# Kernel tuning notes

Hardware: AMD Instinct MI355X
Metric: run time of the kernel (lower is better)

## Reference

```python
import jax, jax.numpy as jnp
import numpy as np

H_SP, W_SP = 8, 8
NUM_HEADS = 6
SHARED = 96
DIM_Q, DIM_KV = 96, 192
WIN = H_SP * W_SP  # 64 tokens per window


def _rel_index():
    # Swin-style relative position index, static numpy computation
    coords = np.stack(np.meshgrid(np.arange(H_SP), np.arange(W_SP), indexing='ij'))
    cf = coords.reshape(2, -1)                      # [2, 64]
    rel = cf[:, :, None] - cf[:, None, :]           # [2, 64, 64]
    rel = rel.transpose(1, 2, 0).astype(np.int64)   # [64, 64, 2]
    rel[..., 0] += H_SP - 1
    rel[..., 1] += W_SP - 1
    rel[..., 0] *= 2 * W_SP - 1
    return rel.sum(-1)                              # [64, 64], values in [0, 225)

REL_IDX = jnp.asarray(_rel_index())


def setup_inputs() -> dict:
    key = jax.random.key(0)
    ks = jax.random.split(key, 12)
    B, H, W = 4, 256, 256
    f32 = jnp.float32
    std = 0.02
    return {
        'x_q':  jax.random.normal(ks[0], (B, DIM_Q, H, W), f32),
        'x_kv': jax.random.normal(ks[1], (B, DIM_KV, H, W), f32),
        'Wq': jax.random.normal(ks[2], (DIM_Q, SHARED), f32) * std,
        'bq': jnp.zeros((SHARED,), f32),
        'Wk': jax.random.normal(ks[3], (DIM_KV, SHARED), f32) * std,
        'bk': jnp.zeros((SHARED,), f32),
        'Wv': jax.random.normal(ks[4], (DIM_KV, SHARED), f32) * std,
        'bv': jnp.zeros((SHARED,), f32),
        'bias_table': jax.random.normal(ks[5], ((2 * H_SP - 1) * (2 * W_SP - 1), NUM_HEADS), f32) * std,
        'Wo': jax.random.normal(ks[6], (SHARED, DIM_Q), f32) * std,
        'bo': jnp.zeros((DIM_Q,), f32),
    }


def reference(x_q, x_kv, Wq, bq, Wk, bk, Wv, bv, bias_table, Wo, bo):
    B, Cq, H, W = x_q.shape
    nH, nW = H // H_SP, W // W_SP  # H, W divisible by window -> pad is a no-op
    hd = SHARED // NUM_HEADS
    scale = hd ** -0.5

    def to_windows(img):
        C = img.shape[1]
        x = img.reshape(B, C, nH, H_SP, nW, W_SP)
        return x.transpose(0, 2, 4, 3, 5, 1).reshape(-1, WIN, C)

    qw = to_windows(x_q)    # [nWin, 64, Cq]
    kvw = to_windows(x_kv)  # [nWin, 64, Ckv]

    def heads(x):
        return x.reshape(-1, WIN, NUM_HEADS, hd).transpose(0, 2, 1, 3)  # [nWin, h, 64, hd]

    q = heads(qw @ Wq + bq)
    k = heads(kvw @ Wk + bk)
    v = heads(kvw @ Wv + bv)

    attn = jnp.einsum('whqd,whkd->whqk', q, k) * scale  # [nWin, h, 64, 64]
    rel_bias = bias_table[REL_IDX].transpose(2, 0, 1)   # [h, 64, 64]
    attn = jax.nn.softmax(attn + rel_bias[None], axis=-1)

    out = jnp.einsum('whqk,whkd->whqd', attn, v)        # [nWin, h, 64, hd]
    out = out.transpose(0, 2, 1, 3).reshape(-1, WIN, SHARED)
    out = out @ Wo + bo                                 # [nWin, 64, Cq]

    # windows2img
    out = out.reshape(B, nH, nW, H_SP, W_SP, Cq)
    out = out.transpose(0, 1, 3, 2, 4, 5).reshape(B, H, W, Cq)
    return out.transpose(0, 3, 1, 2)  # [B, Cq, H, W]
```

## Files before the change

kernel.cpp:

```cpp
#include <hip/hip_runtime.h>

typedef short short8 __attribute__((ext_vector_type(8)));
typedef float f32x4 __attribute__((ext_vector_type(4)));
typedef unsigned short ushort;

#define MFMA(a, b, c) __builtin_amdgcn_mfma_f32_16x16x32_bf16(a, b, c, 0, 0, 0)

#define WS_WQT 0
#define WS_WKT 9216
#define WS_WVT 27648
#define WS_WOT 46080
#define WS_BIAS 55296
#define WS_TOTAL 56646

#define STR_A 104
#define OFF_A 0
#define OFF_K16 13312
#define OFF_VT 25600
#define STR_VT 72
#define OFF_PQ 39424
#define P_STRIDE 72
#define OFF_BIAS 50688
#define LDS_BYTES 53392

__device__ __forceinline__ ushort f2bf(float x) {
    unsigned u = __float_as_uint(x);
    u = (u + 0x7FFFu + ((u >> 16) & 1u)) >> 16;
    return (ushort)u;
}
__device__ __forceinline__ float bf2f(ushort u) {
    return __uint_as_float(((unsigned)u) << 16);
}

__global__ void prep_weights(const float* __restrict__ Wq, const float* __restrict__ Wk,
                             const float* __restrict__ Wv, const float* __restrict__ Wo,
                             const float* __restrict__ btab, ushort* __restrict__ ws) {
    int idx = blockIdx.x * 256 + threadIdx.x;
    if (idx < WS_WKT) {
        int f = idx >> 9, w = idx & 511, lane = w >> 3, j = w & 7;
        int nt = f / 3, kt = f % 3;
        int n = nt * 16 + (lane & 15), k = kt * 32 + (lane >> 4) * 8 + j;
        ws[idx] = f2bf(Wq[k * 96 + n]);
    } else if (idx < WS_WVT) {
        int t = idx - WS_WKT;
        int f = t >> 9, w = t & 511, lane = w >> 3, j = w & 7;
        int kt6 = f / 6, nt = f % 6;
        int n = nt * 16 + (lane & 15), k = kt6 * 32 + (lane >> 4) * 8 + j;
        ws[idx] = f2bf(Wk[k * 96 + n]);
    } else if (idx < WS_WOT) {
        int t = idx - WS_WVT;
        int f = t >> 9, w = t & 511, lane = w >> 3, j = w & 7;
        int kt6 = f / 6, nt = f % 6;
        int n = nt * 16 + (lane & 15), k = kt6 * 32 + (lane >> 4) * 8 + j;
        ws[idx] = f2bf(Wv[k * 96 + n]);
    } else if (idx < WS_BIAS) {
        int t = idx - WS_WOT;
        int f = t >> 9, w = t & 511, lane = w >> 3, j = w & 7;
        int nt = f / 3, kt = f % 3;
        int n = nt * 16 + (lane & 15), k = kt * 32 + (lane >> 4) * 8 + j;
        ws[idx] = f2bf(Wo[k * 96 + n]);
    } else if (idx < WS_TOTAL) {
        ws[idx] = f2bf(btab[idx - WS_BIAS]);
    }
}

__global__ __launch_bounds__(256, 3) void swin_attn(
    const float* __restrict__ xq, const float* __restrict__ xkv,
    const float* __restrict__ bq, const float* __restrict__ bk,
    const float* __restrict__ bv, const float* __restrict__ bo,
    const ushort* __restrict__ ws, float* __restrict__ out)
{
    __shared__ __align__(16) char smem[LDS_BYTES];
    const int tid = threadIdx.x;
    const int wave = tid >> 6, lane = tid & 63;
    const int l15 = lane & 15, quad = lane >> 4;
    int wid = ((blockIdx.x & 7) << 9) | (blockIdx.x >> 3);
    const int b = wid >> 10;
    const int wh = (wid >> 5) & 31, ww = wid & 31;
    const int h0 = wh * 8, w0 = ww * 8;
    const int mt = wave;

    ushort* A     = (ushort*)(smem + OFF_A);
    ushort* k16   = (ushort*)(smem + OFF_K16);
    ushort* vt    = (ushort*)(smem + OFF_VT);
    ushort* ps    = (ushort*)(smem + OFF_PQ) + wave * (16 * P_STRIDE);
    ushort* qsc   = (ushort*)(smem + OFF_PQ + 9216) + wave * 256;
    ushort* biasl = (ushort*)(smem + OFF_BIAS);

    float bqr[6], bkr[6], bvr[6], bor[6];
    #pragma unroll
    for (int h = 0; h < 6; ++h) {
        bqr[h] = bq[h * 16 + l15]; bkr[h] = bk[h * 16 + l15];
        bvr[h] = bv[h * 16 + l15]; bor[h] = bo[h * 16 + l15];
    }

    int pc[3], pi[3];
    #pragma unroll
    for (int t = 0; t < 3; ++t) { int p = tid + t * 256; pc[t] = p % 96; pi[t] = p / 96; }

    const float* xkvb = xkv + (size_t)b * 192 * 65536;
    float4 pf[3][2];
    #pragma unroll
    for (int t = 0; t < 3; ++t) {
        const float* g = xkvb + (size_t)pc[t] * 65536 + (h0 + pi[t]) * 256 + w0;
        pf[t][0] = *(const float4*)g; pf[t][1] = *(const float4*)(g + 4);
    }
    for (int i = tid; i < 1350; i += 256) biasl[i] = ws[WS_BIAS + i];

    #pragma unroll
    for (int t = 0; t < 3; ++t) {
        int base = (pi[t] * 8) * STR_A + pc[t];
        A[base]             = f2bf(pf[t][0].x); A[base + STR_A]     = f2bf(pf[t][0].y);
        A[base + 2 * STR_A] = f2bf(pf[t][0].z); A[base + 3 * STR_A] = f2bf(pf[t][0].w);
        A[base + 4 * STR_A] = f2bf(pf[t][1].x); A[base + 5 * STR_A] = f2bf(pf[t][1].y);
        A[base + 6 * STR_A] = f2bf(pf[t][1].z); A[base + 7 * STR_A] = f2bf(pf[t][1].w);
    }
    __syncthreads();

    float4 pg[3][2];
    #pragma unroll
    for (int t = 0; t < 3; ++t) {
        const float* g = xkvb + (size_t)(96 + pc[t]) * 65536 + (h0 + pi[t]) * 256 + w0;
        pg[t][0] = *(const float4*)g; pg[t][1] = *(const float4*)(g + 4);
    }

    f32x4 accK[6], accV[6];
    #pragma unroll
    for (int n = 0; n < 6; ++n) { accK[n] = {}; accV[n] = {}; }
    const int arow = (mt * 16 + l15) * STR_A + quad * 8;
    #pragma unroll
    for (int kt = 0; kt < 3; ++kt) {
        short8 a = *(const short8*)(A + arow + kt * 32);
        #pragma unroll
        for (int nt = 0; nt < 6; ++nt) {
            short8 bk8 = *(const short8*)(ws + WS_WKT + (((kt * 6) + nt) * 64 + lane) * 8);
            accK[nt] = MFMA(a, bk8, accK[nt]);
            short8 bv8 = *(const short8*)(ws + WS_WVT + (((kt * 6) + nt) * 64 + lane) * 8);
            accV[nt] = MFMA(a, bv8, accV[nt]);
        }
    }
    __syncthreads();

    #pragma unroll
    for (int t = 0; t < 3; ++t) {
        int base = (pi[t] * 8) * STR_A + pc[t];
        A[base]             = f2bf(pg[t][0].x); A[base + STR_A]     = f2bf(pg[t][0].y);
        A[base + 2 * STR_A] = f2bf(pg[t][0].z); A[base + 3 * STR_A] = f2bf(pg[t][0].w);
        A[base + 4 * STR_A] = f2bf(pg[t][1].x); A[base + 5 * STR_A] = f2bf(pg[t][1].y);
        A[base + 6 * STR_A] = f2bf(pg[t][1].z); A[base + 7 * STR_A] = f2bf(pg[t][1].w);
    }
    __syncthreads();

    const float* xqb = xq + (size_t)b * 96 * 65536;
    #pragma unroll
    for (int t = 0; t < 3; ++t) {
        const float* g = xqb + (size_t)pc[t] * 65536 + (h0 + pi[t]) * 256 + w0;
        pf[t][0] = *(const float4*)g; pf[t][1] = *(const float4*)(g + 4);
    }

    #pragma unroll
    for (int kt = 0; kt < 3; ++kt) {
        short8 a = *(const short8*)(A + arow + kt * 32);
        #pragma unroll
        for (int nt = 0; nt < 6; ++nt) {
            short8 bk8 = *(const short8*)(ws + WS_WKT + ((((3 + kt) * 6) + nt) * 64 + lane) * 8);
            accK[nt] = MFMA(a, bk8, accK[nt]);
            short8 bv8 = *(const short8*)(ws + WS_WVT + ((((3 + kt) * 6) + nt) * 64 + lane) * 8);
            accV[nt] = MFMA(a, bv8, accV[nt]);
        }
    }
    #pragma unroll
    for (int nt = 0; nt < 6; ++nt) {
        ushort* dk = k16 + nt * (64 * 16) + (mt * 16 + quad * 4) * 16 + l15;
        ushort* dv = vt + nt * (16 * STR_VT) + l15 * STR_VT + (mt * 16 + quad * 4);
        #pragma unroll
        for (int r = 0; r < 4; ++r) {
            dk[r * 16] = f2bf(accK[nt][r] + bkr[nt]);
            dv[r]      = f2bf(accV[nt][r] + bvr[nt]);
        }
    }
    __syncthreads();

    #pragma unroll
    for (int t = 0; t < 3; ++t) {
        int base = (pi[t] * 8) * STR_A + pc[t];
        A[base]             = f2bf(pf[t][0].x); A[base + STR_A]     = f2bf(pf[t][0].y);
        A[base + 2 * STR_A] = f2bf(pf[t][0].z); A[base + 3 * STR_A] = f2bf(pf[t][0].w);
        A[base + 4 * STR_A] = f2bf(pf[t][1].x); A[base + 5 * STR_A] = f2bf(pf[t][1].y);
        A[base + 6 * STR_A] = f2bf(pf[t][1].z); A[base + 7 * STR_A] = f2bf(pf[t][1].w);
    }
    __syncthreads();

    const int qtok0 = mt * 16 + quad * 4;
    int bidx[4][4];
    #pragma unroll
    for (int nt = 0; nt < 4; ++nt) {
        int kt2 = nt * 16 + l15, i2 = kt2 >> 3, j2 = kt2 & 7;
        #pragma unroll
        for (int r = 0; r < 4; ++r) {
            int qt = qtok0 + r, i1 = qt >> 3, j1 = qt & 7;
            bidx[nt][r] = ((i1 - i2 + 7) * 15 + (j1 - j2 + 7)) * 6;
        }
    }

    f32x4 accO[6];
    short8 zero8 = {};
    for (int h = 0; h < 6; ++h) {
        f32x4 qa = {};
        #pragma unroll
        for (int kt = 0; kt < 3; ++kt) {
            short8 a  = *(const short8*)(A + arow + kt * 32);
            short8 bb = *(const short8*)(ws + WS_WQT + ((h * 3 + kt) * 64 + lane) * 8);
            qa = MFMA(a, bb, qa);
        }
        #pragma unroll
        for (int r = 0; r < 4; ++r)
            qsc[(quad * 4 + r) * 16 + l15] = f2bf((qa[r] + bqr[h]) * 0.25f);

        short8 aq = zero8;
        if (quad < 2) aq = *(const short8*)(qsc + l15 * 16 + quad * 8);
        f32x4 s[4];
        #pragma unroll
        for (int nt = 0; nt < 4; ++nt) {
            short8 bk8 = zero8;
            if (quad < 2) bk8 = *(const short8*)(k16 + h * (64 * 16) + (nt * 16 + l15) * 16 + quad * 8);
            f32x4 z = {};
            s[nt] = MFMA(aq, bk8, z);
        }
        #pragma unroll
        for (int nt = 0; nt < 4; ++nt)
            #pragma unroll
            for (int r = 0; r < 4; ++r)
                s[nt][r] += bf2f(biasl[bidx[nt][r] + h]);
        float pr[4][4];
        #pragma unroll
        for (int r = 0; r < 4; ++r) {
            float m = fmaxf(fmaxf(s[0][r], s[1][r]), fmaxf(s[2][r], s[3][r]));
            m = fmaxf(m, __shfl_xor(m, 1)); m = fmaxf(m, __shfl_xor(m, 2));
            m = fmaxf(m, __shfl_xor(m, 4)); m = fmaxf(m, __shfl_xor(m, 8));
            float l = 0.f;
            #pragma unroll
            for (int nt = 0; nt < 4; ++nt) { pr[nt][r] = __expf(s[nt][r] - m); l += pr[nt][r]; }
            l += __shfl_xor(l, 1); l += __shfl_xor(l, 2);
            l += __shfl_xor(l, 4); l += __shfl_xor(l, 8);
            float inv = 1.0f / l;
            #pragma unroll
            for (int nt = 0; nt < 4; ++nt) pr[nt][r] *= inv;
        }
        #pragma unroll
        for (int nt = 0; nt < 4; ++nt)
            #pragma unroll
            for (int r = 0; r < 4; ++r)
                ps[(quad * 4 + r) * P_STRIDE + nt * 16 + l15] = f2bf(pr[nt][r]);
        f32x4 o = {};
        #pragma unroll
        for (int k2 = 0; k2 < 2; ++k2) {
            short8 ap  = *(const short8*)(ps + l15 * P_STRIDE + k2 * 32 + quad * 8);
            short8 bv8 = *(const short8*)(vt + h * (16 * STR_VT) + l15 * STR_VT + k2 * 32 + quad * 8);
            o = MFMA(ap, bv8, o);
        }
        accO[h] = o;
    }
    __syncthreads();

    ushort* obuf = A;
    #pragma unroll
    for (int h = 0; h < 6; ++h)
        #pragma unroll
        for (int r = 0; r < 4; ++r)
            obuf[(mt * 16 + quad * 4 + r) * STR_A + h * 16 + l15] = f2bf(accO[h][r]);

    {
        int t0 = mt * 16 + quad * 4;
        int i = t0 >> 3, j0 = t0 & 7;
        #pragma unroll
        for (int nt = 0; nt < 6; ++nt) {
            f32x4 acc = {};
            #pragma unroll
            for (int kt = 0; kt < 3; ++kt) {
                short8 a  = *(const short8*)(obuf + arow + kt * 32);
                short8 bb = *(const short8*)(ws + WS_WOT + ((nt * 3 + kt) * 64 + lane) * 8);
                acc = MFMA(a, bb, acc);
            }
            int cout = nt * 16 + l15;
            float4 v4 = make_float4(acc[0] + bor[nt], acc[1] + bor[nt], acc[2] + bor[nt], acc[3] + bor[nt]);
            float* dst = out + (size_t)(b * 96 + cout) * 65536 + (h0 + i) * 256 + w0 + j0;
            *(float4*)dst = v4;
        }
    }
}

extern "C" void kernel_launch(void* const* d_in, const int* in_sizes, int n_in,
                              void* d_out, int out_size, void* d_ws, size_t ws_size,
                              hipStream_t stream) {
    const float* xq   = (const float*)d_in[0];
    const float* xkv  = (const float*)d_in[1];
    const float* Wq   = (const float*)d_in[2];
    const float* bq   = (const float*)d_in[3];
    const float* Wk   = (const float*)d_in[4];
    const float* bk   = (const float*)d_in[5];
    const float* Wv   = (const float*)d_in[6];
    const float* bv   = (const float*)d_in[7];
    const float* btab = (const float*)d_in[8];
    const float* Wo   = (const float*)d_in[9];
    const float* bo   = (const float*)d_in[10];
    ushort* ws = (ushort*)d_ws;
    float* out = (float*)d_out;

    hipLaunchKernelGGL(prep_weights, dim3((WS_TOTAL + 255) / 256), dim3(256), 0, stream,
                       Wq, Wk, Wv, Wo, btab, ws);
    hipLaunchKernelGGL(swin_attn, dim3(4096), dim3(256), 0, stream,
                       xq, xkv, bq, bk, bv, bo, ws, out);
}
```

Baseline: 507.7 us.

## Compute Q projection first into registers and shrink LDS to raise occupancy

Reorders the per-window pipeline so the Q projection is done first and held packed in registers. K is then stored in the reused A buffer rather than a separate K tile, which cuts LDS per block from about 53 KB to about 39 KB, and launch bounds are raised to 4 blocks per CU. Biases are folded into the MFMA accumulator initialisation, softmax reductions use DPP instead of shuffles, and rcp replaces the division. The costs are 12 extra live registers for the packed Q under a tighter register budget, and more bank pressure on the strided K reads.

```diff
diff --git a/kernel.cpp b/kernel.cpp
--- a/kernel.cpp
+++ b/kernel.cpp
@@ -14,14 +14,14 @@
 #define WS_TOTAL 56646
 
 #define STR_A 104
-#define OFF_A 0
-#define OFF_K16 13312
-#define OFF_VT 25600
+#define U_A    0
+#define U_VT   6656
 #define STR_VT 72
-#define OFF_PQ 39424
-#define P_STRIDE 72
-#define OFF_BIAS 50688
-#define LDS_BYTES 53392
+#define U_PS   13568
+#define U_BIAS 18176
+#define U_TOTAL 19526
+
+#define DPP_F(v, ctrl) __int_as_float(__builtin_amdgcn_update_dpp(0, __float_as_int(v), ctrl, 0xF, 0xF, true))
 
 __device__ __forceinline__ ushort f2bf(float x) {
     unsigned u = __float_as_uint(x);
@@ -64,13 +64,13 @@
     }
 }
 
-__global__ __launch_bounds__(256, 3) void swin_attn(
+__global__ __launch_bounds__(256, 4) void swin_attn(
     const float* __restrict__ xq, const float* __restrict__ xkv,
     const float* __restrict__ bq, const float* __restrict__ bk,
     const float* __restrict__ bv, const float* __restrict__ bo,
     const ushort* __restrict__ ws, float* __restrict__ out)
 {
-    __shared__ __align__(16) char smem[LDS_BYTES];
+    __shared__ __align__(16) ushort smem[U_TOTAL + 8];
     const int tid = threadIdx.x;
     const int wave = tid >> 6, lane = tid & 63;
     const int l15 = lane & 15, quad = lane >> 4;
@@ -80,29 +80,27 @@
     const int h0 = wh * 8, w0 = ww * 8;
     const int mt = wave;
 
-    ushort* A     = (ushort*)(smem + OFF_A);
-    ushort* k16   = (ushort*)(smem + OFF_K16);
-    ushort* vt    = (ushort*)(smem + OFF_VT);
-    ushort* ps    = (ushort*)(smem + OFF_PQ) + wave * (16 * P_STRIDE);
-    ushort* qsc   = (ushort*)(smem + OFF_PQ + 9216) + wave * 256;
-    ushort* biasl = (ushort*)(smem + OFF_BIAS);
-
-    float bqr[6], bkr[6], bvr[6], bor[6];
+    ushort* A     = smem + U_A;
+    ushort* vt    = smem + U_VT;
+    ushort* ps    = smem + U_PS + wave * 1152;
+    ushort* qsc   = ps;
+    ushort* biasl = smem + U_BIAS;
+
+    float bqr[6], bkr[6], bvr[6];
     #pragma unroll
     for (int h = 0; h < 6; ++h) {
-        bqr[h] = bq[h * 16 + l15]; bkr[h] = bk[h * 16 + l15];
-        bvr[h] = bv[h * 16 + l15]; bor[h] = bo[h * 16 + l15];
+        bqr[h] = bq[h * 16 + l15]; bkr[h] = bk[h * 16 + l15]; bvr[h] = bv[h * 16 + l15];
     }
 
     int pc[3], pi[3];
     #pragma unroll
     for (int t = 0; t < 3; ++t) { int p = tid + t * 256; pc[t] = p % 96; pi[t] = p / 96; }
 
-    const float* xkvb = xkv + (size_t)b * 192 * 65536;
+    const float* xqb = xq + (size_t)b * 96 * 65536;
     float4 pf[3][2];
     #pragma unroll
     for (int t = 0; t < 3; ++t) {
-        const float* g = xkvb + (size_t)pc[t] * 65536 + (h0 + pi[t]) * 256 + w0;
+        const float* g = xqb + (size_t)pc[t] * 65536 + (h0 + pi[t]) * 256 + w0;
         pf[t][0] = *(const float4*)g; pf[t][1] = *(const float4*)(g + 4);
     }
     for (int i = tid; i < 1350; i += 256) biasl[i] = ws[WS_BIAS + i];
@@ -117,17 +115,52 @@
     }
     __syncthreads();
 
+    const float* xkvb = xkv + (size_t)b * 192 * 65536;
     float4 pg[3][2];
     #pragma unroll
     for (int t = 0; t < 3; ++t) {
+        const float* g = xkvb + (size_t)pc[t] * 65536 + (h0 + pi[t]) * 256 + w0;
+        pg[t][0] = *(const float4*)g; pg[t][1] = *(const float4*)(g + 4);
+    }
+
+    const int arow = (mt * 16 + l15) * STR_A + quad * 8;
+    short8 a0 = *(const short8*)(A + arow);
+    short8 a1 = *(const short8*)(A + arow + 32);
+    short8 a2 = *(const short8*)(A + arow + 64);
+    unsigned qpk[12];
+    #pragma unroll
+    for (int h = 0; h < 6; ++h) {
+        f32x4 qa = {bqr[h], bqr[h], bqr[h], bqr[h]};
+        qa = MFMA(a0, *(const short8*)(ws + WS_WQT + ((h * 3 + 0) * 64 + lane) * 8), qa);
+        qa = MFMA(a1, *(const short8*)(ws + WS_WQT + ((h * 3 + 1) * 64 + lane) * 8), qa);
+        qa = MFMA(a2, *(const short8*)(ws + WS_WQT + ((h * 3 + 2) * 64 + lane) * 8), qa);
+        qpk[h * 2]     = (unsigned)f2bf(qa[0] * 0.25f) | ((unsigned)f2bf(qa[1] * 0.25f) << 16);
+        qpk[h * 2 + 1] = (unsigned)f2bf(qa[2] * 0.25f) | ((unsigned)f2bf(qa[3] * 0.25f) << 16);
+    }
+    __syncthreads();
+
+    #pragma unroll
+    for (int t = 0; t < 3; ++t) {
+        int base = (pi[t] * 8) * STR_A + pc[t];
+        A[base]             = f2bf(pg[t][0].x); A[base + STR_A]     = f2bf(pg[t][0].y);
+        A[base + 2 * STR_A] = f2bf(pg[t][0].z); A[base + 3 * STR_A] = f2bf(pg[t][0].w);
+        A[base + 4 * STR_A] = f2bf(pg[t][1].x); A[base + 5 * STR_A] = f2bf(pg[t][1].y);
+        A[base + 6 * STR_A] = f2bf(pg[t][1].z); A[base + 7 * STR_A] = f2bf(pg[t][1].w);
+    }
+    __syncthreads();
+
+    #pragma unroll
+    for (int t = 0; t < 3; ++t) {
         const float* g = xkvb + (size_t)(96 + pc[t]) * 65536 + (h0 + pi[t]) * 256 + w0;
-        pg[t][0] = *(const float4*)g; pg[t][1] = *(const float4*)(g + 4);
+        pf[t][0] = *(const float4*)g; pf[t][1] = *(const float4*)(g + 4);
     }
 
     f32x4 accK[6], accV[6];
     #pragma unroll
-    for (int n = 0; n < 6; ++n) { accK[n] = {}; accV[n] = {}; }
-    const int arow = (mt * 16 + l15) * STR_A + quad * 8;
+    for (int n = 0; n < 6; ++n) {
+        accK[n] = {bkr[n], bkr[n], bkr[n], bkr[n]};
+        accV[n] = {bvr[n], bvr[n], bvr[n], bvr[n]};
+    }
     #pragma unroll
     for (int kt = 0; kt < 3; ++kt) {
         short8 a = *(const short8*)(A + arow + kt * 32);
@@ -144,19 +177,12 @@
     #pragma unroll
     for (int t = 0; t < 3; ++t) {
         int base = (pi[t] * 8) * STR_A + pc[t];
-        A[base]             = f2bf(pg[t][0].x); A[base + STR_A]     = f2bf(pg[t][0].y);
-        A[base + 2 * STR_A] = f2bf(pg[t][0].z); A[base + 3 * STR_A] = f2bf(pg[t][0].w);
-        A[base + 4 * STR_A] = f2bf(pg[t][1].x); A[base + 5 * STR_A] = f2bf(pg[t][1].y);
-        A[base + 6 * STR_A] = f2bf(pg[t][1].z); A[base + 7 * STR_A] = f2bf(pg[t][1].w);
-    }
-    __syncthreads();
-
-    const float* xqb = xq + (size_t)b * 96 * 65536;
-    #pragma unroll
-    for (int t = 0; t < 3; ++t) {
-        const float* g = xqb + (size_t)pc[t] * 65536 + (h0 + pi[t]) * 256 + w0;
-        pf[t][0] = *(const float4*)g; pf[t][1] = *(const float4*)(g + 4);
-    }
+        A[base]             = f2bf(pf[t][0].x); A[base + STR_A]     = f2bf(pf[t][0].y);
+        A[base + 2 * STR_A] = f2bf(pf[t][0].z); A[base + 3 * STR_A] = f2bf(pf[t][0].w);
+        A[base + 4 * STR_A] = f2bf(pf[t][1].x); A[base + 5 * STR_A] = f2bf(pf[t][1].y);
+        A[base + 6 * STR_A] = f2bf(pf[t][1].z); A[base + 7 * STR_A] = f2bf(pf[t][1].w);
+    }
+    __syncthreads();
 
     #pragma unroll
     for (int kt = 0; kt < 3; ++kt) {
@@ -171,23 +197,13 @@
     }
     #pragma unroll
     for (int nt = 0; nt < 6; ++nt) {
-        ushort* dk = k16 + nt * (64 * 16) + (mt * 16 + quad * 4) * 16 + l15;
+        ushort* dk = A + (mt * 16 + quad * 4) * STR_A + nt * 16 + l15;
         ushort* dv = vt + nt * (16 * STR_VT) + l15 * STR_VT + (mt * 16 + quad * 4);
         #pragma unroll
         for (int r = 0; r < 4; ++r) {
-            dk[r * 16] = f2bf(accK[nt][r] + bkr[nt]);
-            dv[r]      = f2bf(accV[nt][r] + bvr[nt]);
-        }
-    }
-    __syncthreads();
-
-    #pragma unroll
-    for (int t = 0; t < 3; ++t) {
-        int base = (pi[t] * 8) * STR_A + pc[t];
-        A[base]             = f2bf(pf[t][0].x); A[base + STR_A]     = f2bf(pf[t][0].y);
-        A[base + 2 * STR_A] = f2bf(pf[t][0].z); A[base + 3 * STR_A] = f2bf(pf[t][0].w);
-        A[base + 4 * STR_A] = f2bf(pf[t][1].x); A[base + 5 * STR_A] = f2bf(pf[t][1].y);
-        A[base + 6 * STR_A] = f2bf(pf[t][1].z); A[base + 7 * STR_A] = f2bf(pf[t][1].w);
+            dk[r * STR_A] = f2bf(accK[nt][r]);
+            dv[r]         = f2bf(accV[nt][r]);
+        }
     }
     __syncthreads();
 
@@ -205,57 +221,52 @@
 
     f32x4 accO[6];
     short8 zero8 = {};
+    #pragma unroll
     for (int h = 0; h < 6; ++h) {
-        f32x4 qa = {};
-        #pragma unroll
-        for (int kt = 0; kt < 3; ++kt) {
-            short8 a  = *(const short8*)(A + arow + kt * 32);
-            short8 bb = *(const short8*)(ws + WS_WQT + ((h * 3 + kt) * 64 + lane) * 8);
-            qa = MFMA(a, bb, qa);
-        }
-        #pragma unroll
-        for (int r = 0; r < 4; ++r)
-            qsc[(quad * 4 + r) * 16 + l15] = f2bf((qa[r] + bqr[h]) * 0.25f);
-
+        asm volatile("" ::: "memory");
+        unsigned wlo = qpk[h * 2], whi = qpk[h * 2 + 1];
+        qsc[(quad * 4 + 0) * 24 + l15] = (ushort)wlo;
+        qsc[(quad * 4 + 1) * 24 + l15] = (ushort)(wlo >> 16);
+        qsc[(quad * 4 + 2) * 24 + l15] = (ushort)whi;
+        qsc[(quad * 4 + 3) * 24 + l15] = (ushort)(whi >> 16);
         short8 aq = zero8;
-        if (quad < 2) aq = *(const short8*)(qsc + l15 * 16 + quad * 8);
+        if (quad < 2) aq = *(const short8*)(qsc + l15 * 24 + quad * 8);
         f32x4 s[4];
         #pragma unroll
         for (int nt = 0; nt < 4; ++nt) {
             short8 bk8 = zero8;
-            if (quad < 2) bk8 = *(const short8*)(k16 + h * (64 * 16) + (nt * 16 + l15) * 16 + quad * 8);
-            f32x4 z = {};
-            s[nt] = MFMA(aq, bk8, z);
+            if (quad < 2) bk8 = *(const short8*)(A + (nt * 16 + l15) * STR_A + h * 16 + quad * 8);
+            f32x4 c;
+            c[0] = bf2f(biasl[bidx[nt][0] + h]); c[1] = bf2f(biasl[bidx[nt][1] + h]);
+            c[2] = bf2f(biasl[bidx[nt][2] + h]); c[3] = bf2f(biasl[bidx[nt][3] + h]);
+            s[nt] = MFMA(aq, bk8, c);
+        }
+        float pr[4][4];
+        #pragma unroll
+        for (int r = 0; r < 4; ++r) {
+            float m = fmaxf(fmaxf(s[0][r], s[1][r]), fmaxf(s[2][r], s[3][r]));
+            m = fmaxf(m, DPP_F(m, 0xB1));
+            m = fmaxf(m, DPP_F(m, 0x4E));
+            m = fmaxf(m, DPP_F(m, 0x124));
+            m = fmaxf(m, DPP_F(m, 0x128));
+            float l = 0.f;
+            #pragma unroll
+            for (int nt = 0; nt < 4; ++nt) { pr[nt][r] = __expf(s[nt][r] - m); l += pr[nt][r]; }
+            l += DPP_F(l, 0xB1); l += DPP_F(l, 0x4E);
+            l += DPP_F(l, 0x124); l += DPP_F(l, 0x128);
+            float inv = __builtin_amdgcn_rcpf(l);
+            #pragma unroll
+            for (int nt = 0; nt < 4; ++nt) pr[nt][r] *= inv;
         }
         #pragma unroll
         for (int nt = 0; nt < 4; ++nt)
             #pragma unroll
             for (int r = 0; r < 4; ++r)
-                s[nt][r] += bf2f(biasl[bidx[nt][r] + h]);
-        float pr[4][4];
-        #pragma unroll
-        for (int r = 0; r < 4; ++r) {
-            float m = fmaxf(fmaxf(s[0][r], s[1][r]), fmaxf(s[2][r], s[3][r]));
-            m = fmaxf(m, __shfl_xor(m, 1)); m = fmaxf(m, __shfl_xor(m, 2));
-            m = fmaxf(m, __shfl_xor(m, 4)); m = fmaxf(m, __shfl_xor(m, 8));
-            float l = 0.f;
-            #pragma unroll
-            for (int nt = 0; nt < 4; ++nt) { pr[nt][r] = __expf(s[nt][r] - m); l += pr[nt][r]; }
-            l += __shfl_xor(l, 1); l += __shfl_xor(l, 2);
-            l += __shfl_xor(l, 4); l += __shfl_xor(l, 8);
-            float inv = 1.0f / l;
-            #pragma unroll
-            for (int nt = 0; nt < 4; ++nt) pr[nt][r] *= inv;
-        }
-        #pragma unroll
-        for (int nt = 0; nt < 4; ++nt)
-            #pragma unroll
-            for (int r = 0; r < 4; ++r)
-                ps[(quad * 4 + r) * P_STRIDE + nt * 16 + l15] = f2bf(pr[nt][r]);
+                ps[(quad * 4 + r) * 72 + nt * 16 + l15] = f2bf(pr[nt][r]);
         f32x4 o = {};
         #pragma unroll
         for (int k2 = 0; k2 < 2; ++k2) {
-            short8 ap  = *(const short8*)(ps + l15 * P_STRIDE + k2 * 32 + quad * 8);
+            short8 ap  = *(const short8*)(ps + l15 * 72 + k2 * 32 + quad * 8);
             short8 bv8 = *(const short8*)(vt + h * (16 * STR_VT) + l15 * STR_VT + k2 * 32 + quad * 8);
             o = MFMA(ap, bv8, o);
         }
@@ -263,6 +274,9 @@
     }
     __syncthreads();
 
+    float bor_[6];
+    #pragma unroll
+    for (int h = 0; h < 6; ++h) bor_[h] = bo[h * 16 + l15];
     ushort* obuf = A;
     #pragma unroll
     for (int h = 0; h < 6; ++h)
@@ -275,7 +289,7 @@
         int i = t0 >> 3, j0 = t0 & 7;
         #pragma unroll
         for (int nt = 0; nt < 6; ++nt) {
-            f32x4 acc = {};
+            f32x4 acc = {bor_[nt], bor_[nt], bor_[nt], bor_[nt]};
             #pragma unroll
             for (int kt = 0; kt < 3; ++kt) {
                 short8 a  = *(const short8*)(obuf + arow + kt * 32);
@@ -283,7 +297,7 @@
                 acc = MFMA(a, bb, acc);
             }
             int cout = nt * 16 + l15;
-            float4 v4 = make_float4(acc[0] + bor[nt], acc[1] + bor[nt], acc[2] + bor[nt], acc[3] + bor[nt]);
+            float4 v4 = make_float4(acc[0], acc[1], acc[2], acc[3]);
             float* dst = out + (size_t)(b * 96 + cout) * 65536 + (h0 + i) * 256 + w0 + j0;
             *(float4*)dst = v4;
         }
```

After: 505.2 us. Within noise of the previous version (-0.5%).
